# Kernel optimization log

Measured on AMD Instinct MI355X. Metric: run time of the kernel, lower is better.

The kernel has to match this reference:

```python
import jax, jax.numpy as jnp
import numpy as np

B, T, C, H = 4, 2048, 1024, 16
HD = C // H  # head dim = 64


def setup_inputs() -> dict:
    key = jax.random.key(0)
    k1, k2, k3, k4, k5 = jax.random.split(key, 5)
    s_in = 1.0 / np.sqrt(C)
    return {
        "x": jax.random.normal(k1, (B, T, C), dtype=jnp.float32),
        "W_attn": jax.random.uniform(k2, (C, 3 * C), dtype=jnp.float32, minval=-s_in, maxval=s_in),
        "b_attn": jax.random.uniform(k3, (3 * C,), dtype=jnp.float32, minval=-s_in, maxval=s_in),
        "W_proj": jax.random.uniform(k4, (C, C), dtype=jnp.float32, minval=-s_in, maxval=s_in),
        "b_proj": jax.random.uniform(k5, (C,), dtype=jnp.float32, minval=-s_in, maxval=s_in),
    }


def reference(x, W_attn, b_attn, W_proj, b_proj):
    Bx, Tx, Cx = x.shape
    qkv = x @ W_attn + b_attn                      # [B,T,3C]
    q, k, v = jnp.split(qkv, 3, axis=2)
    # [B,T,C] -> [B,H,T,HD]
    def heads(t):
        return t.reshape(Bx, Tx, H, HD).transpose(0, 2, 1, 3)
    q, k, v = heads(q), heads(k), heads(v)
    scale = 1.0 / np.sqrt(HD).astype(np.float32)
    att = jnp.einsum('bhqd,bhkd->bhqk', q, k) * scale
    causal = jnp.tril(jnp.ones((Tx, Tx), dtype=bool))
    att = jnp.where(causal[None, None], att, -jnp.inf)
    att = jax.nn.softmax(att, axis=-1)
    y = jnp.einsum('bhqk,bhkd->bhqd', att, v)      # [B,H,T,HD]
    y = y.transpose(0, 2, 1, 3).reshape(Bx, Tx, Cx)
    return y @ W_proj + b_proj
```

## Files before the change

kernel.cpp:

```cpp
#include <hip/hip_runtime.h>
#include <math.h>

#define Bn 4
#define Tn 2048
#define Cn 1024
#define Hn 16
#define HDn 64
#define Mn (Bn * Tn)

typedef unsigned short u16;
typedef unsigned int u32;
typedef __attribute__((ext_vector_type(8))) short bf16x8;
typedef __attribute__((ext_vector_type(8))) unsigned short us8;
typedef __attribute__((ext_vector_type(4))) float f32x4;
typedef __attribute__((ext_vector_type(16))) float f32x16;
typedef __attribute__((ext_vector_type(4))) unsigned int u32x4;

__device__ __forceinline__ float b2f(u16 u) {
    return __uint_as_float(((u32)u) << 16);
}
__device__ __forceinline__ u16 f2b(float f) {
    u32 u = __float_as_uint(f);
    return (u16)((u + 0x7FFFu + ((u >> 16) & 1u)) >> 16);
}
__device__ __forceinline__ u32 cvtpk(float a, float b) {
    u32 d;
    asm("v_cvt_pk_bf16_f32 %0, %1, %2" : "=v"(d) : "v"(a), "v"(b));
    return d;
}
__device__ __forceinline__ void pswap(u32& a, u32& b) {
    asm("v_permlane32_swap_b32 %0, %1" : "+v"(a), "+v"(b));
}

__device__ __forceinline__ int xcd_work(int bid, int nwg) {
    return (bid & 7) * (nwg >> 3) + (bid >> 3);
}

#define GLL(srcp, dstp)                                                     \
    __builtin_amdgcn_global_load_lds(                                       \
        (const __attribute__((address_space(1))) u32*)(srcp),               \
        (__attribute__((address_space(3))) u32*)(dstp), 16, 0, 0)

#define WAITCNT4() asm volatile("s_waitcnt vmcnt(4)" ::: "memory")
#define WAITCNT0() asm volatile("s_waitcnt vmcnt(0)" ::: "memory")

__global__ __launch_bounds__(256) void cvt_f32_bf16_kernel(
    const float4* __restrict__ in, ushort4* __restrict__ out, int n4)
{
    for (int i = blockIdx.x * 256 + threadIdx.x; i < n4; i += gridDim.x * 256) {
        float4 v = in[i];
        ushort4 o;
        o.x = f2b(v.x); o.y = f2b(v.y); o.z = f2b(v.z); o.w = f2b(v.w);
        out[i] = o;
    }
}

__global__ __launch_bounds__(256) void transpose_cvt_kernel(
    const float* __restrict__ in, u16* __restrict__ out, int R, int Cc)
{
    __shared__ u16 t[32][33];
    const int c0 = blockIdx.x * 32, r0 = blockIdx.y * 32;
    const int tx = threadIdx.x & 31, ty = threadIdx.x >> 5;
    #pragma unroll
    for (int i = 0; i < 32; i += 8)
        t[ty + i][tx] = f2b(in[(size_t)(r0 + ty + i) * Cc + c0 + tx]);
    __syncthreads();
    #pragma unroll
    for (int i = 0; i < 32; i += 8)
        out[(size_t)(c0 + ty + i) * R + r0 + tx] = t[tx][ty + i];
}

template <bool OUT_BF16, bool QKV_MODE>
__global__ __launch_bounds__(256) void gemm_bf16_kernel(
    const u16* __restrict__ A, const u16* __restrict__ BT,
    const float* __restrict__ bias,
    u16* __restrict__ outb, float* __restrict__ outf, u16* __restrict__ vTout,
    int N, int K, int nx)
{
    __shared__ u16 Al[3][128 * 32];
    __shared__ u16 Bl[3][128 * 32];

    const int tid = threadIdx.x;
    const int workid = xcd_work(blockIdx.x, gridDim.x);
    const int brow = (workid / nx) * 128;
    const int bcol = (workid % nx) * 128;
    const int w  = tid >> 6;
    const int wr = w >> 1, wc = w & 1;
    const int l  = tid & 63;
    const int lr = l & 15;
    const int lk = (l >> 4) << 3;

    const int r0s = tid >> 2,            c0s = (tid & 3) << 3;
    const int r1s = (256 + tid) >> 2;
    const int d0s = (tid & 192) * 8;
    const int d1s = (256 + (tid & 192)) * 8;

    f32x4 acc[4][4];
    #pragma unroll
    for (int m = 0; m < 4; ++m)
        #pragma unroll
        for (int n = 0; n < 4; ++n) acc[m][n] = (f32x4){0.f, 0.f, 0.f, 0.f};

    #define STAGE_G(k0, bufi)                                                \
        do {                                                                 \
            GLL(&A [(size_t)(brow + r0s) * K + (k0) + c0s], &Al[bufi][d0s]); \
            GLL(&BT[(size_t)(bcol + r0s) * K + (k0) + c0s], &Bl[bufi][d0s]); \
            GLL(&A [(size_t)(brow + r1s) * K + (k0) + c0s], &Al[bufi][d1s]); \
            GLL(&BT[(size_t)(bcol + r1s) * K + (k0) + c0s], &Bl[bufi][d1s]); \
        } while (0)

    const int T = K >> 5;
    STAGE_G(0, 0);
    STAGE_G(32, 1);

    int cur = 0;
    for (int t = 0; t < T; ++t) {
        if (t < T - 1) WAITCNT4();
        else           WAITCNT0();
        __builtin_amdgcn_s_barrier();

        if (t + 2 < T) {
            const int nb = cur + 2 >= 3 ? cur - 1 : cur + 2;
            STAGE_G((t + 2) << 5, nb);
        }

        bf16x8 a[4], b[4];
        #pragma unroll
        for (int m = 0; m < 4; ++m)
            a[m] = *(const bf16x8*)&Al[cur][(wr * 64 + m * 16 + lr) * 32 + lk];
        #pragma unroll
        for (int n = 0; n < 4; ++n)
            b[n] = *(const bf16x8*)&Bl[cur][(wc * 64 + n * 16 + lr) * 32 + lk];

        __builtin_amdgcn_s_setprio(1);
        #pragma unroll
        for (int m = 0; m < 4; ++m)
            #pragma unroll
            for (int n = 0; n < 4; ++n)
                acc[m][n] = __builtin_amdgcn_mfma_f32_16x16x32_bf16(
                    a[m], b[n], acc[m][n], 0, 0, 0);
        __builtin_amdgcn_s_setprio(0);

        cur = cur == 2 ? 0 : cur + 1;
    }
    #undef STAGE_G

    const int orow0 = brow + wr * 64 + ((l >> 4) << 2);
    const int ocol0 = bcol + wc * 64 + lr;
    if (QKV_MODE && bcol >= 2048) {
        #pragma unroll
        for (int n = 0; n < 4; ++n) {
            const int c = ocol0 + n * 16 - 2048;
            const float bv = bias[ocol0 + n * 16];
            #pragma unroll
            for (int m = 0; m < 4; ++m) {
                const int row0 = orow0 + m * 16;
                const int bb = row0 >> 11, t0 = row0 & 2047;
                ushort4 pk;
                pk.x = f2b(acc[m][n][0] + bv);
                pk.y = f2b(acc[m][n][1] + bv);
                pk.z = f2b(acc[m][n][2] + bv);
                pk.w = f2b(acc[m][n][3] + bv);
                *(ushort4*)&vTout[((size_t)bb * Cn + c) * Tn + t0] = pk;
            }
        }
    } else {
        #pragma unroll
        for (int n = 0; n < 4; ++n) {
            const int col = ocol0 + n * 16;
            const float bv = bias[col];
            #pragma unroll
            for (int m = 0; m < 4; ++m) {
                #pragma unroll
                for (int r = 0; r < 4; ++r) {
                    const int row = orow0 + m * 16 + r;
                    const float v = acc[m][n][r] + bv;
                    if (OUT_BF16) outb[(size_t)row * N + col] = f2b(v);
                    else          outf[(size_t)row * N + col] = v;
                }
            }
        }
    }
}

__global__ __launch_bounds__(256, 2) void attn_mfma7_kernel(
    const u16* __restrict__ qkvb, const u16* __restrict__ vT,
    u16* __restrict__ yb)
{
    __shared__ u16 Kb[3][64 * 64];
    __shared__ u16 Vb[3][64 * 64];

    const int tid = threadIdx.x;
    const int w   = tid >> 6;
    const int l   = tid & 63;
    const int q31 = l & 31;
    const int hi  = l >> 5;
    const int work = xcd_work(blockIdx.x, 512);
    const int pr  = work & 7;
    const int bh  = work >> 3;
    const int b   = bh >> 4, h = bh & 15;

    const float S2 = 0.18033688f;

    const u16* Kg = qkvb + (size_t)(b * Tn) * (3 * Cn) + Cn + h * HDn;
    const u16* Vg = vT + (size_t)bh * HDn * Tn;

    const int srow = l >> 3;
    const int schk = ((l & 7) ^ srow) << 3;
    const int rloc = w * 16;
    const int rsw8 = q31 & 7;

    #define STAGE_A(kt, bufi)                                                  \
        do {                                                                   \
            _Pragma("unroll")                                                  \
            for (int jc = 0; jc < 2; ++jc) {                                   \
                const int rr = rloc + jc * 8;                                  \
                GLL(Kg + (size_t)((kt) * 64 + rr + srow) * (3 * Cn) + schk,    \
                    &Kb[bufi][rr * 64]);                                       \
                GLL(Vg + (size_t)(rr + srow) * Tn + (kt) * 64 + schk,          \
                    &Vb[bufi][rr * 64]);                                       \
            }                                                                  \
        } while (0)

    #pragma unroll 1
    for (int half = 0; half < 2; ++half) {
        const int qt = half ? (15 - pr) : pr;
        const int ktmax = 2 * qt + 2;
        const int qrow0 = qt * 128 + w * 32;
        const int qglob = qrow0 + q31;

        const u16* Qp = qkvb + (size_t)(b * Tn + qglob) * (3 * Cn)
                        + h * HDn + hi * 8;
        bf16x8 qf[4];
        #pragma unroll
        for (int c = 0; c < 4; ++c) qf[c] = *(const bf16x8*)(Qp + c * 16);

        f32x16 O0, O1;
        #pragma unroll
        for (int r = 0; r < 16; ++r) { O0[r] = 0.f; O1[r] = 0.f; }
        float m = -INFINITY, ls = 0.f;

        STAGE_A(0, 0);
        STAGE_A(1, 1);

        int cur = 0;
        for (int kt = 0; kt < ktmax; ++kt) {
            if (kt < ktmax - 1) WAITCNT4();
            else                WAITCNT0();
            __builtin_amdgcn_s_barrier();

            if (kt + 2 < ktmax) {
                const int nb = cur + 2 >= 3 ? cur - 1 : cur + 2;
                STAGE_A(kt + 2, nb);
            }
            const u16* Kc = Kb[cur];
            const u16* Vc = Vb[cur];

            if (kt * 64 <= qrow0 + 31) {
                f32x16 S0, S1;
                #pragma unroll
                for (int r = 0; r < 16; ++r) { S0[r] = 0.f; S1[r] = 0.f; }
                __builtin_amdgcn_s_setprio(1);
                #pragma unroll
                for (int c = 0; c < 4; ++c) {
                    const int co = ((2 * c + hi) ^ rsw8) << 3;
                    const bf16x8 k0 = *(const bf16x8*)&Kc[q31 * 64 + co];
                    const bf16x8 k1 = *(const bf16x8*)&Kc[(32 + q31) * 64 + co];
                    S0 = __builtin_amdgcn_mfma_f32_32x32x16_bf16(k0, qf[c], S0, 0, 0, 0);
                    S1 = __builtin_amdgcn_mfma_f32_32x32x16_bf16(k1, qf[c], S1, 0, 0, 0);
                }
                __builtin_amdgcn_s_setprio(0);

                if (kt * 64 + 63 > qrow0) {
                    #pragma unroll
                    for (int r = 0; r < 16; ++r) {
                        const int kl = kt * 64 + (r & 3) + 8 * (r >> 2) + 4 * hi;
                        if (kl > qglob)      S0[r] = -INFINITY;
                        if (kl + 32 > qglob) S1[r] = -INFINITY;
                    }
                }

                float mt = S0[0];
                #pragma unroll
                for (int r = 1; r < 16; ++r) mt = fmaxf(mt, S0[r]);
                #pragma unroll
                for (int r = 0; r < 16; ++r) mt = fmaxf(mt, S1[r]);
                mt = fmaxf(mt, __shfl_xor(mt, 32));

                float lscale = 1.f;
                if (__any(mt > m + 64.f)) {
                    const float mn = fmaxf(m, mt);
                    const float alpha = exp2f((m - mn) * S2);
                    m = mn; lscale = alpha;
                    #pragma unroll
                    for (int r = 0; r < 16; ++r) {
                        const int qloc = (r & 3) + 8 * (r >> 2) + 4 * hi;
                        const float ar = __shfl(alpha, qloc);
                        O0[r] *= ar; O1[r] *= ar;
                    }
                }

                float lt = 0.f;
                u32 w0[8], w1[8];
                #pragma unroll
                for (int i = 0; i < 8; ++i) {
                    const float p0 = exp2f((S0[2 * i]     - m) * S2);
                    const float p1 = exp2f((S0[2 * i + 1] - m) * S2);
                    const float p2 = exp2f((S1[2 * i]     - m) * S2);
                    const float p3 = exp2f((S1[2 * i + 1] - m) * S2);
                    lt += (p0 + p1) + (p2 + p3);
                    w0[i] = cvtpk(p0, p1);
                    w1[i] = cvtpk(p2, p3);
                }
                lt += __shfl_xor(lt, 32);
                ls = ls * lscale + lt;

                __builtin_amdgcn_s_setprio(1);
                #pragma unroll
                for (int t2 = 0; t2 < 2; ++t2) {
                    #pragma unroll
                    for (int c1 = 0; c1 < 2; ++c1) {
                        u32 a0 = t2 ? w1[4 * c1 + 0] : w0[4 * c1 + 0];
                        u32 b0 = t2 ? w1[4 * c1 + 2] : w0[4 * c1 + 2];
                        u32 a1 = t2 ? w1[4 * c1 + 1] : w0[4 * c1 + 1];
                        u32 b1 = t2 ? w1[4 * c1 + 3] : w0[4 * c1 + 3];
                        pswap(a0, b0);
                        pswap(a1, b1);
                        u32x4 fr; fr.x = a0; fr.y = a1; fr.z = b0; fr.w = b1;
                        const bf16x8 pf = __builtin_bit_cast(bf16x8, fr);
                        const int c = t2 * 2 + c1;
                        const int co = ((2 * c + hi) ^ rsw8) << 3;
                        const bf16x8 v0 = *(const bf16x8*)&Vc[q31 * 64 + co];
                        const bf16x8 v1 = *(const bf16x8*)&Vc[(32 + q31) * 64 + co];
                        O0 = __builtin_amdgcn_mfma_f32_32x32x16_bf16(pf, v0, O0, 0, 0, 0);
                        O1 = __builtin_amdgcn_mfma_f32_32x32x16_bf16(pf, v1, O1, 0, 0, 0);
                    }
                }
                __builtin_amdgcn_s_setprio(0);
            }

            cur = cur == 2 ? 0 : cur + 1;
        }

        __builtin_amdgcn_s_barrier();

        #pragma unroll
        for (int r = 0; r < 16; ++r) {
            const int qloc = (r & 3) + 8 * (r >> 2) + 4 * hi;
            const float inv = __builtin_amdgcn_rcpf(__shfl(ls, qloc));
            u16* yp = yb + (size_t)(b * Tn + qrow0 + qloc) * Cn + h * HDn + q31;
            yp[0]  = f2b(O0[r] * inv);
            yp[32] = f2b(O1[r] * inv);
        }
    }
    #undef STAGE_A
}

extern "C" void kernel_launch(void* const* d_in, const int* in_sizes, int n_in,
                              void* d_out, int out_size, void* d_ws, size_t ws_size,
                              hipStream_t stream)
{
    const float* x      = (const float*)d_in[0];
    const float* W_attn = (const float*)d_in[1];
    const float* b_attn = (const float*)d_in[2];
    const float* W_proj = (const float*)d_in[3];
    const float* b_proj = (const float*)d_in[4];
    float* out = (float*)d_out;

    u16* xb   = (u16*)d_ws;
    u16* WaT  = xb   + (size_t)Mn * Cn;
    u16* WpT  = WaT  + (size_t)3 * Cn * Cn;
    u16* qkvb = WpT  + (size_t)Cn * Cn;
    u16* yb   = qkvb + (size_t)Mn * 3 * Cn;
    u16* vT   = yb   + (size_t)Mn * Cn;

    cvt_f32_bf16_kernel<<<2048, 256, 0, stream>>>(
        (const float4*)x, (ushort4*)xb, Mn * Cn / 4);

    transpose_cvt_kernel<<<dim3(3 * Cn / 32, Cn / 32), 256, 0, stream>>>(
        W_attn, WaT, Cn, 3 * Cn);
    transpose_cvt_kernel<<<dim3(Cn / 32, Cn / 32), 256, 0, stream>>>(
        W_proj, WpT, Cn, Cn);

    gemm_bf16_kernel<true, true><<<24 * 64, 256, 0, stream>>>(
        xb, WaT, b_attn, qkvb, nullptr, vT, 3 * Cn, Cn, 24);

    attn_mfma7_kernel<<<512, 256, 0, stream>>>(qkvb, vT, yb);

    gemm_bf16_kernel<false, false><<<8 * 64, 256, 0, stream>>>(
        yb, WpT, b_proj, nullptr, out, nullptr, Cn, Cn, 8);
}
```

Baseline: 200.9 us.

## Load GEMM A operand directly from global and streamline attention softmax math

The GEMM kernel stops staging the A tile in LDS and has each wave read its A fragments straight from global memory. Only B is prefetched through LDS, with occupancy raised to 4 blocks per CU and sched barriers pinning the order of the loads. In attention, the row max uses v_max3 trees, exp2 calls go to the raw hardware intrinsic with an fma-folded argument, and the row sum is split into two accumulators. The direct A loads skip LDS traffic and barriers but may expose global latency and duplicate A reads across the two column waves.

Measured after the change: 233.0 us. +16.0%, slower.

```diff
diff --git a/kernel.cpp b/kernel.cpp
--- a/kernel.cpp
+++ b/kernel.cpp
@@ -31,6 +31,12 @@
 __device__ __forceinline__ void pswap(u32& a, u32& b) {
     asm("v_permlane32_swap_b32 %0, %1" : "+v"(a), "+v"(b));
 }
+__device__ __forceinline__ float max3f(float a, float b, float c) {
+    float d;
+    asm("v_max3_f32 %0, %1, %2, %3" : "=v"(d) : "v"(a), "v"(b), "v"(c));
+    return d;
+}
+#define EXP2R(x) __builtin_amdgcn_exp2f(x)
 
 __device__ __forceinline__ int xcd_work(int bid, int nwg) {
     return (bid & 7) * (nwg >> 3) + (bid >> 3);
@@ -41,6 +47,7 @@
         (const __attribute__((address_space(1))) u32*)(srcp),               \
         (__attribute__((address_space(3))) u32*)(dstp), 16, 0, 0)
 
+#define WAITCNT2() asm volatile("s_waitcnt vmcnt(2)" ::: "memory")
 #define WAITCNT4() asm volatile("s_waitcnt vmcnt(4)" ::: "memory")
 #define WAITCNT0() asm volatile("s_waitcnt vmcnt(0)" ::: "memory")
 
@@ -71,13 +78,12 @@
 }
 
 template <bool OUT_BF16, bool QKV_MODE>
-__global__ __launch_bounds__(256) void gemm_bf16_kernel(
+__global__ __launch_bounds__(256, 4) void gemm_ag_kernel(
     const u16* __restrict__ A, const u16* __restrict__ BT,
     const float* __restrict__ bias,
     u16* __restrict__ outb, float* __restrict__ outf, u16* __restrict__ vTout,
     int N, int K, int nx)
 {
-    __shared__ u16 Al[3][128 * 32];
     __shared__ u16 Bl[3][128 * 32];
 
     const int tid = threadIdx.x;
@@ -90,10 +96,8 @@
     const int lr = l & 15;
     const int lk = (l >> 4) << 3;
 
-    const int r0s = tid >> 2,            c0s = (tid & 3) << 3;
-    const int r1s = (256 + tid) >> 2;
-    const int d0s = (tid & 192) * 8;
-    const int d1s = (256 + (tid & 192)) * 8;
+    const int srow = l >> 2;
+    const int schk = (l & 3) << 3;
 
     f32x4 acc[4][4];
     #pragma unroll
@@ -101,49 +105,53 @@
         #pragma unroll
         for (int n = 0; n < 4; ++n) acc[m][n] = (f32x4){0.f, 0.f, 0.f, 0.f};
 
-    #define STAGE_G(k0, bufi)                                                \
-        do {                                                                 \
-            GLL(&A [(size_t)(brow + r0s) * K + (k0) + c0s], &Al[bufi][d0s]); \
-            GLL(&BT[(size_t)(bcol + r0s) * K + (k0) + c0s], &Bl[bufi][d0s]); \
-            GLL(&A [(size_t)(brow + r1s) * K + (k0) + c0s], &Al[bufi][d1s]); \
-            GLL(&BT[(size_t)(bcol + r1s) * K + (k0) + c0s], &Bl[bufi][d1s]); \
+    #define STAGE_B(k0, bufi)                                                  \
+        do {                                                                   \
+            GLL(&BT[(size_t)(bcol +      w * 16 + srow) * K + (k0) + schk],    \
+                &Bl[bufi][(w * 16) * 32]);                                     \
+            GLL(&BT[(size_t)(bcol + 64 + w * 16 + srow) * K + (k0) + schk],    \
+                &Bl[bufi][(64 + w * 16) * 32]);                                \
         } while (0)
 
     const int T = K >> 5;
-    STAGE_G(0, 0);
-    STAGE_G(32, 1);
+    STAGE_B(0, 0);
+    STAGE_B(32, 1);
+
+    const u16* Arow = A + (size_t)(brow + wr * 64 + lr) * K + lk;
 
     int cur = 0;
     for (int t = 0; t < T; ++t) {
-        if (t < T - 1) WAITCNT4();
-        else           WAITCNT0();
+        WAITCNT2();
         __builtin_amdgcn_s_barrier();
 
+        const int k0 = t << 5;
+        bf16x8 a[4];
+        #pragma unroll
+        for (int m = 0; m < 4; ++m)
+            a[m] = *(const bf16x8*)(Arow + (size_t)(m * 16) * K + k0);
+
+        bf16x8 b[4];
+        #pragma unroll
+        for (int n = 0; n < 4; ++n)
+            b[n] = *(const bf16x8*)&Bl[cur][(wc * 64 + n * 16 + lr) * 32 + lk];
+
+        __builtin_amdgcn_sched_barrier(0);
         if (t + 2 < T) {
             const int nb = cur + 2 >= 3 ? cur - 1 : cur + 2;
-            STAGE_G((t + 2) << 5, nb);
+            STAGE_B((t + 2) << 5, nb);
         }
-
-        bf16x8 a[4], b[4];
-        #pragma unroll
-        for (int m = 0; m < 4; ++m)
-            a[m] = *(const bf16x8*)&Al[cur][(wr * 64 + m * 16 + lr) * 32 + lk];
-        #pragma unroll
-        for (int n = 0; n < 4; ++n)
-            b[n] = *(const bf16x8*)&Bl[cur][(wc * 64 + n * 16 + lr) * 32 + lk];
-
-        __builtin_amdgcn_s_setprio(1);
+        __builtin_amdgcn_sched_barrier(0);
+
         #pragma unroll
         for (int m = 0; m < 4; ++m)
             #pragma unroll
             for (int n = 0; n < 4; ++n)
                 acc[m][n] = __builtin_amdgcn_mfma_f32_16x16x32_bf16(
                     a[m], b[n], acc[m][n], 0, 0, 0);
-        __builtin_amdgcn_s_setprio(0);
 
         cur = cur == 2 ? 0 : cur + 1;
     }
-    #undef STAGE_G
+    #undef STAGE_B
 
     const int orow0 = brow + wr * 64 + ((l >> 4) << 2);
     const int ocol0 = bcol + wc * 64 + lr;
@@ -183,7 +191,7 @@
     }
 }
 
-__global__ __launch_bounds__(256, 2) void attn_mfma7_kernel(
+__global__ __launch_bounds__(256, 2) void attn_mfma8_kernel(
     const u16* __restrict__ qkvb, const u16* __restrict__ vT,
     u16* __restrict__ yb)
 {
@@ -280,17 +288,28 @@
                     }
                 }
 
-                float mt = S0[0];
-                #pragma unroll
-                for (int r = 1; r < 16; ++r) mt = fmaxf(mt, S0[r]);
-                #pragma unroll
-                for (int r = 0; r < 16; ++r) mt = fmaxf(mt, S1[r]);
+                float a0 = max3f(S0[0],  S0[1],  S0[2]);
+                float a1 = max3f(S0[3],  S0[4],  S0[5]);
+                float a2 = max3f(S0[6],  S0[7],  S0[8]);
+                float a3 = max3f(S0[9],  S0[10], S0[11]);
+                float a4 = max3f(S0[12], S0[13], S0[14]);
+                float a5 = max3f(S0[15], S1[0],  S1[1]);
+                float a6 = max3f(S1[2],  S1[3],  S1[4]);
+                float a7 = max3f(S1[5],  S1[6],  S1[7]);
+                float a8 = max3f(S1[8],  S1[9],  S1[10]);
+                float a9 = max3f(S1[11], S1[12], S1[13]);
+                float aA = fmaxf(S1[14], S1[15]);
+                float b0 = max3f(a0, a1, a2);
+                float b1 = max3f(a3, a4, a5);
+                float b2 = max3f(a6, a7, a8);
+                float b3 = fmaxf(a9, aA);
+                float mt = fmaxf(fmaxf(b0, b1), fmaxf(b2, b3));
                 mt = fmaxf(mt, __shfl_xor(mt, 32));
 
                 float lscale = 1.f;
                 if (__any(mt > m + 64.f)) {
                     const float mn = fmaxf(m, mt);
-                    const float alpha = exp2f((m - mn) * S2);
+                    const float alpha = EXP2R((m - mn) * S2);
                     m = mn; lscale = alpha;
                     #pragma unroll
                     for (int r = 0; r < 16; ++r) {
@@ -300,18 +319,21 @@
                     }
                 }
 
-                float lt = 0.f;
+                const float nms2 = -m * S2;
+                float lt0 = 0.f, lt1 = 0.f;
                 u32 w0[8], w1[8];
                 #pragma unroll
                 for (int i = 0; i < 8; ++i) {
-                    const float p0 = exp2f((S0[2 * i]     - m) * S2);
-                    const float p1 = exp2f((S0[2 * i + 1] - m) * S2);
-                    const float p2 = exp2f((S1[2 * i]     - m) * S2);
-                    const float p3 = exp2f((S1[2 * i + 1] - m) * S2);
-                    lt += (p0 + p1) + (p2 + p3);
+                    const float p0 = EXP2R(fmaf(S0[2 * i],     S2, nms2));
+                    const float p1 = EXP2R(fmaf(S0[2 * i + 1], S2, nms2));
+                    const float p2 = EXP2R(fmaf(S1[2 * i],     S2, nms2));
+                    const float p3 = EXP2R(fmaf(S1[2 * i + 1], S2, nms2));
+                    lt0 += (p0 + p1);
+                    lt1 += (p2 + p3);
                     w0[i] = cvtpk(p0, p1);
                     w1[i] = cvtpk(p2, p3);
                 }
+                float lt = lt0 + lt1;
                 lt += __shfl_xor(lt, 32);
                 ls = ls * lscale + lt;
 
@@ -320,13 +342,13 @@
                 for (int t2 = 0; t2 < 2; ++t2) {
                     #pragma unroll
                     for (int c1 = 0; c1 < 2; ++c1) {
-                        u32 a0 = t2 ? w1[4 * c1 + 0] : w0[4 * c1 + 0];
-                        u32 b0 = t2 ? w1[4 * c1 + 2] : w0[4 * c1 + 2];
-                        u32 a1 = t2 ? w1[4 * c1 + 1] : w0[4 * c1 + 1];
-                        u32 b1 = t2 ? w1[4 * c1 + 3] : w0[4 * c1 + 3];
-                        pswap(a0, b0);
-                        pswap(a1, b1);
-                        u32x4 fr; fr.x = a0; fr.y = a1; fr.z = b0; fr.w = b1;
+                        u32 a0w = t2 ? w1[4 * c1 + 0] : w0[4 * c1 + 0];
+                        u32 b0w = t2 ? w1[4 * c1 + 2] : w0[4 * c1 + 2];
+                        u32 a1w = t2 ? w1[4 * c1 + 1] : w0[4 * c1 + 1];
+                        u32 b1w = t2 ? w1[4 * c1 + 3] : w0[4 * c1 + 3];
+                        pswap(a0w, b0w);
+                        pswap(a1w, b1w);
+                        u32x4 fr; fr.x = a0w; fr.y = a1w; fr.z = b0w; fr.w = b1w;
                         const bf16x8 pf = __builtin_bit_cast(bf16x8, fr);
                         const int c = t2 * 2 + c1;
                         const int co = ((2 * c + hi) ^ rsw8) << 3;
@@ -382,11 +404,11 @@
     transpose_cvt_kernel<<<dim3(Cn / 32, Cn / 32), 256, 0, stream>>>(
         W_proj, WpT, Cn, Cn);
 
-    gemm_bf16_kernel<true, true><<<24 * 64, 256, 0, stream>>>(
+    gemm_ag_kernel<true, true><<<64 * 24, 256, 0, stream>>>(
         xb, WaT, b_attn, qkvb, nullptr, vT, 3 * Cn, Cn, 24);
 
-    attn_mfma7_kernel<<<512, 256, 0, stream>>>(qkvb, vT, yb);
-
-    gemm_bf16_kernel<false, false><<<8 * 64, 256, 0, stream>>>(
+    attn_mfma8_kernel<<<512, 256, 0, stream>>>(qkvb, vT, yb);
+
+    gemm_ag_kernel<false, false><<<64 * 8, 256, 0, stream>>>(
         yb, WpT, b_proj, nullptr, out, nullptr, Cn, Cn, 8);
 }
```
